# Kernel tuning notes

Measured on AMD Instinct MI355X. Metric: run time of the kernel, lower is better.

## Reference

```python
import jax, jax.numpy as jnp
import numpy as np

CH = 128
GROUPS = 8
EPS = 1e-5

def group_norm(x, w, b):
    B, C, H, W = x.shape
    g = x.reshape(B, GROUPS, C // GROUPS, H, W)
    mean = g.mean(axis=(2, 3, 4), keepdims=True)
    var = g.var(axis=(2, 3, 4), keepdims=True)
    g = (g - mean) * jax.lax.rsqrt(var + EPS)
    g = g.reshape(B, C, H, W)
    return g * w[None, :, None, None] + b[None, :, None, None]

def setup_inputs() -> dict:
    key = jax.random.key(0)
    ks = jax.random.split(key, 7)
    C = CH
    x = jax.random.normal(ks[0], (8, C, 64, 64), dtype=jnp.float32)
    gn_w = jnp.ones((C,), dtype=jnp.float32)
    gn_b = jnp.zeros((C,), dtype=jnp.float32)
    s = 1.0 / np.sqrt(C)
    qkv_w = jax.random.normal(ks[1], (3 * C, C), dtype=jnp.float32) * s
    qkv_b = jax.random.normal(ks[2], (3 * C,), dtype=jnp.float32) * 0.01
    proj_w = jax.random.normal(ks[3], (C, C), dtype=jnp.float32) * s
    proj_b = jax.random.normal(ks[4], (C,), dtype=jnp.float32) * 0.01
    return {"x": x, "gn_w": gn_w, "gn_b": gn_b, "qkv_w": qkv_w,
            "qkv_b": qkv_b, "proj_w": proj_w, "proj_b": proj_b}

def reference(x, gn_w, gn_b, qkv_w, qkv_b, proj_w, proj_b):
    B, C, H, W = x.shape
    h = group_norm(x, gn_w, gn_b)
    # 1x1 conv == per-pixel matmul over channels
    qkv = jnp.einsum('bchw,oc->bohw', h, qkv_w) + qkv_b[None, :, None, None]
    q, k, v = jnp.split(qkv.reshape(B, 3 * C, H * W), 3, axis=1)  # each [B,C,N]
    scale = C ** (-0.5)
    attn = jax.nn.softmax(jnp.einsum('bci,bcj->bij', q * scale, k), axis=-1)
    out = jnp.einsum('bij,bcj->bci', attn, v).reshape(B, C, H, W)
    out = jnp.einsum('bchw,oc->bohw', out, proj_w) + proj_b[None, :, None, None]
    return x + out
```

## Files before the change

### kernel.cpp

```cpp
#include <hip/hip_runtime.h>
#include <stdint.h>


typedef __attribute__((ext_vector_type(8))) short short8;
typedef __attribute__((ext_vector_type(4))) float f32x4;
typedef __attribute__((ext_vector_type(16))) float f32x16;

#define MFMA_BF16(a, b, c) __builtin_amdgcn_mfma_f32_16x16x32_bf16((a), (b), (c), 0, 0, 0)
#define MFMA32(a, b, c) __builtin_amdgcn_mfma_f32_32x32x16_bf16((a), (b), (c), 0, 0, 0)
#define EXP2(x) __builtin_amdgcn_exp2f(x)

#define QSCALE 0.12751743f

__device__ __forceinline__ unsigned short f2bf(float f) {
    unsigned int u = __builtin_bit_cast(unsigned int, f);
    u += 0x7FFFu + ((u >> 16) & 1u);
    return (unsigned short)(u >> 16);
}
__device__ __forceinline__ float bf2f(unsigned int lo16) {
    return __builtin_bit_cast(float, lo16 << 16);
}
__device__ __forceinline__ short8 ldg8(const unsigned short* p) {
    return __builtin_bit_cast(short8, *(const uint4*)p);
}

__global__ __launch_bounds__(256) void k_pre(const float* __restrict__ x,
                                             float* __restrict__ sums,
                                             const float* __restrict__ qkv_w,
                                             const float* __restrict__ proj_w,
                                             unsigned short* __restrict__ wq,
                                             unsigned short* __restrict__ wp) {
    if (blockIdx.x >= 1024) {
        int i = ((blockIdx.x - 1024) * 256 + threadIdx.x) * 4;
        const float* src; unsigned short* dst; int off;
        if (i < 49152) { src = qkv_w; dst = wq; off = i; }
        else           { src = proj_w; dst = wp; off = i - 49152; }
        float4 v = *(const float4*)(src + off);
        uint2 pk;
        pk.x = (unsigned int)f2bf(v.x) | ((unsigned int)f2bf(v.y) << 16);
        pk.y = (unsigned int)f2bf(v.z) | ((unsigned int)f2bf(v.w) << 16);
        *(uint2*)(dst + off) = pk;
        return;
    }
    int g     = blockIdx.x >> 4;
    int slice = blockIdx.x & 15;
    const float* p = x + (size_t)g * 65536 + slice * 4096;
    float s = 0.f, sq = 0.f;
#pragma unroll
    for (int i = 0; i < 4; ++i) {
        float4 v = *(const float4*)(p + threadIdx.x * 4 + i * 1024);
        s  += v.x + v.y + v.z + v.w;
        sq += v.x*v.x + v.y*v.y + v.z*v.z + v.w*v.w;
    }
#pragma unroll
    for (int m = 1; m < 64; m <<= 1) { s += __shfl_xor(s, m, 64); sq += __shfl_xor(sq, m, 64); }
    __shared__ float ss[4], ssq[4];
    int w = threadIdx.x >> 6;
    if ((threadIdx.x & 63) == 0) { ss[w] = s; ssq[w] = sq; }
    __syncthreads();
    if (threadIdx.x == 0) {
        atomicAdd(&sums[g * 2],     ss[0] + ss[1] + ss[2] + ss[3]);
        atomicAdd(&sums[g * 2 + 1], ssq[0] + ssq[1] + ssq[2] + ssq[3]);
    }
}

__global__ __launch_bounds__(256) void k_qkv(const float* __restrict__ x,
                                             const float* __restrict__ sums,
                                             const float* __restrict__ gn_w,
                                             const float* __restrict__ gn_b,
                                             const unsigned short* __restrict__ wq,
                                             const float* __restrict__ qkv_b,
                                             unsigned short* __restrict__ q_ws,
                                             unsigned short* __restrict__ k_ws,
                                             unsigned short* __restrict__ v_ws) {
    __shared__ unsigned short h_lds[64][136];
    const int tid  = threadIdx.x;
    const int b    = blockIdx.x >> 6;
    const int n0   = (blockIdx.x & 63) << 6;
    const int lane = tid & 63, wave = tid >> 6;
    const int l15  = lane & 15, q4 = lane >> 4;

    {
        int cb = tid >> 4;
        int nn = (tid & 15) << 2;
#pragma unroll
        for (int k = 0; k < 8; ++k) {
            int c = cb + (k << 4);
            float4 v = *(const float4*)(x + ((size_t)(b * 128 + c) << 12) + n0 + nn);
            int g = c >> 4;
            float ts = sums[(b * 8 + g) * 2];
            float tq = sums[(b * 8 + g) * 2 + 1];
            float mean = ts * (1.f / 65536.f);
            float var  = tq * (1.f / 65536.f) - mean * mean;
            float rstd = rsqrtf(var + 1e-5f);
            float ga = gn_w[c] * rstd;
            float be = gn_b[c] - mean * ga;
            h_lds[nn + 0][c] = f2bf(v.x * ga + be);
            h_lds[nn + 1][c] = f2bf(v.y * ga + be);
            h_lds[nn + 2][c] = f2bf(v.z * ga + be);
            h_lds[nn + 3][c] = f2bf(v.w * ga + be);
        }
    }
    __syncthreads();

    short8 bfrag[4][4];
#pragma unroll
    for (int nt = 0; nt < 4; ++nt)
#pragma unroll
        for (int ks = 0; ks < 4; ++ks)
            bfrag[nt][ks] = *(const short8*)&h_lds[nt * 16 + l15][ks * 32 + q4 * 8];

#pragma unroll
    for (int ot = 0; ot < 6; ++ot) {
        int o0 = wave * 96 + ot * 16;
        short8 af[4];
#pragma unroll
        for (int ks = 0; ks < 4; ++ks)
            af[ks] = ldg8(wq + (size_t)(o0 + l15) * 128 + ks * 32 + q4 * 8);

        if (o0 < 256) {
            float bias[4];
#pragma unroll
            for (int r = 0; r < 4; ++r) bias[r] = qkv_b[o0 + q4 * 4 + r];
            float qs = (o0 < 128) ? QSCALE : 1.0f;
#pragma unroll
            for (int nt = 0; nt < 4; ++nt) {
                f32x4 acc = {0.f, 0.f, 0.f, 0.f};
#pragma unroll
                for (int ks = 0; ks < 4; ++ks)
                    acc = MFMA_BF16(af[ks], bfrag[nt][ks], acc);
                int n = n0 + nt * 16 + l15;
                unsigned short* dst = (o0 < 128) ? q_ws : k_ws;
                int oo = (o0 < 128) ? o0 : (o0 - 128);
                unsigned int lo = (unsigned int)f2bf((acc[0] + bias[0]) * qs) |
                                  ((unsigned int)f2bf((acc[1] + bias[1]) * qs) << 16);
                unsigned int hi = (unsigned int)f2bf((acc[2] + bias[2]) * qs) |
                                  ((unsigned int)f2bf((acc[3] + bias[3]) * qs) << 16);
                uint2 pk; pk.x = lo; pk.y = hi;
                *(uint2*)&dst[((size_t)(b * 4096 + n) << 7) + oo + q4 * 4] = pk;
            }
        } else {
            int c = o0 - 256 + l15;
            float vb = qkv_b[o0 + l15];
            unsigned short* vrow = v_ws + ((size_t)(b * 128 + c) << 12) + n0;
#pragma unroll
            for (int nt = 0; nt < 4; ++nt) {
                f32x4 acc = {0.f, 0.f, 0.f, 0.f};
#pragma unroll
                for (int ks = 0; ks < 4; ++ks)
                    acc = MFMA_BF16(bfrag[nt][ks], af[ks], acc);
                unsigned int lo = (unsigned int)f2bf(acc[0] + vb) |
                                  ((unsigned int)f2bf(acc[1] + vb) << 16);
                unsigned int hi = (unsigned int)f2bf(acc[2] + vb) |
                                  ((unsigned int)f2bf(acc[3] + vb) << 16);
                uint2 pk; pk.x = lo; pk.y = hi;
                *(uint2*)&vrow[nt * 16 + q4 * 4] = pk;
            }
        }
    }
}

__global__ __launch_bounds__(256, 3) void k_attn_part(const unsigned short* __restrict__ q_ws,
                                                      const unsigned short* __restrict__ k_ws,
                                                      const unsigned short* __restrict__ v_ws,
                                                      unsigned short* __restrict__ o_part,
                                                      float* __restrict__ ml) {
    __shared__ unsigned short K_lds[64][136];
    __shared__ unsigned short V_lds[128][72];
    __shared__ unsigned short P_lds[64][72];

    const int tid   = threadIdx.x;
    const int chunk = blockIdx.x & 3;
    const int tile  = (blockIdx.x >> 2) & 63;
    const int b     = blockIdx.x >> 8;
    const int i0    = tile << 6;
    const int lane  = tid & 63, wave = tid >> 6;
    const int ih    = wave >> 1, jh = wave & 1;
    const int l31   = lane & 31, h = lane >> 5;

    const short8 ones = {(short)0x3F80, (short)0x3F80, (short)0x3F80, (short)0x3F80,
                         (short)0x3F80, (short)0x3F80, (short)0x3F80, (short)0x3F80};

    short8 qf[8];
    {
        const unsigned short* qp =
            q_ws + ((size_t)(b * 4096 + i0 + ih * 32 + l31) << 7) + h * 8;
#pragma unroll
        for (int ks = 0; ks < 8; ++ks) qf[ks] = ldg8(qp + ks * 16);
    }

    f32x16 acc[2];
    f32x16 lacc;
#pragma unroll
    for (int e = 0; e < 16; ++e) { lacc[e] = 0.f; acc[0][e] = 0.f; acc[1][e] = 0.f; }

    const unsigned short* kbase = k_ws + ((size_t)b << 19);
    const unsigned short* vsrc  = v_ws + ((size_t)b << 19) +
                                  ((size_t)(tid >> 1) << 12) + (tid & 1) * 32;

    for (int it = 0; it < 16; ++it) {
        int j0 = (chunk << 10) + (it << 6);
        __syncthreads();
        {
            const unsigned short* ksrc = kbase + ((size_t)j0 << 7);
#pragma unroll
            for (int i = 0; i < 4; ++i) {
                int f = i * 256 + tid;
                int row = f >> 4, q = (f & 15) << 3;
                *(uint4*)&K_lds[row][q] = *(const uint4*)(ksrc + f * 8);
            }
            const unsigned short* vp = vsrc + j0;
            uint4* vd = (uint4*)&V_lds[tid >> 1][(tid & 1) * 32];
#pragma unroll
            for (int k = 0; k < 4; ++k) vd[k] = *(const uint4*)(vp + k * 8);
        }
        __syncthreads();

        f32x16 s;
#pragma unroll
        for (int e = 0; e < 16; ++e) s[e] = 0.f;
#pragma unroll
        for (int ks = 0; ks < 8; ++ks) {
            short8 kf = *(const short8*)&K_lds[jh * 32 + l31][ks * 16 + h * 8];
            s = MFMA32(kf, qf[ks], s);
        }

        unsigned short* prow = &P_lds[ih * 32 + l31][jh * 32 + (h << 2)];
#pragma unroll
        for (int rr = 0; rr < 4; ++rr) {
            unsigned int lo = (unsigned int)f2bf(EXP2(fminf(s[rr * 4 + 0], 30.f))) |
                              ((unsigned int)f2bf(EXP2(fminf(s[rr * 4 + 1], 30.f))) << 16);
            unsigned int hi = (unsigned int)f2bf(EXP2(fminf(s[rr * 4 + 2], 30.f))) |
                              ((unsigned int)f2bf(EXP2(fminf(s[rr * 4 + 3], 30.f))) << 16);
            uint2 pk; pk.x = lo; pk.y = hi;
            *(uint2*)(prow + rr * 8) = pk;
        }
        __syncthreads();

#pragma unroll
        for (int ks = 0; ks < 4; ++ks) {
            short8 pf = *(const short8*)&P_lds[ih * 32 + l31][ks * 16 + h * 8];
            lacc = MFMA32(pf, ones, lacc);
#pragma unroll
            for (int ct = 0; ct < 2; ++ct) {
                short8 vf = *(const short8*)&V_lds[jh * 64 + ct * 32 + l31][ks * 16 + h * 8];
                acc[ct] = MFMA32(pf, vf, acc[ct]);
            }
        }
    }

    size_t pbase = (size_t)((b * 64 + tile) * 4 + chunk) * 8192;
    float rl[16];
#pragma unroll
    for (int r = 0; r < 16; ++r) rl[r] = 1.0f / lacc[r];
#pragma unroll
    for (int ct = 0; ct < 2; ++ct)
#pragma unroll
        for (int r = 0; r < 16; ++r) {
            int row = ih * 32 + (r & 3) + ((r >> 2) << 3) + (h << 2);
            o_part[pbase + (size_t)row * 128 + jh * 64 + ct * 32 + l31] =
                f2bf(acc[ct][r] * rl[r]);
        }
    if (l31 == 0 && jh == 0) {
        int mb = ((b * 64 + tile) * 4 + chunk) * 64;
#pragma unroll
        for (int r = 0; r < 16; ++r)
            ml[mb + ih * 32 + (r & 3) + ((r >> 2) << 3) + (h << 2)] = __log2f(lacc[r]);
    }
}

__global__ __launch_bounds__(256) void k_merge_proj(const unsigned short* __restrict__ o_part,
                                                    const float* __restrict__ ml,
                                                    const float* __restrict__ x,
                                                    const unsigned short* __restrict__ wp,
                                                    const float* __restrict__ proj_b,
                                                    float* __restrict__ out) {
    __shared__ unsigned short O_lds[64][136];
    __shared__ float wgt[64][4];
    const int tid  = threadIdx.x;
    const int b    = blockIdx.x >> 6;
    const int tile = blockIdx.x & 63;
    const int i0   = tile << 6;
    const int lane = tid & 63, wave = tid >> 6;
    const int l15  = lane & 15, q4 = lane >> 4;
    const int tb   = (b * 64 + tile) * 4;

    if (tid < 64) {
        float m0 = ml[(tb + 0) * 64 + tid], m1 = ml[(tb + 1) * 64 + tid];
        float m2 = ml[(tb + 2) * 64 + tid], m3 = ml[(tb + 3) * 64 + tid];
        float M = fmaxf(fmaxf(m0, m1), fmaxf(m2, m3));
        float w0 = EXP2(m0 - M), w1 = EXP2(m1 - M), w2 = EXP2(m2 - M), w3 = EXP2(m3 - M);
        float rW = 1.0f / (w0 + w1 + w2 + w3);
        wgt[tid][0] = w0 * rW; wgt[tid][1] = w1 * rW;
        wgt[tid][2] = w2 * rW; wgt[tid][3] = w3 * rW;
    }
    __syncthreads();

    {
        int n = tid >> 2, q = tid & 3;
        float w[4];
#pragma unroll
        for (int ch = 0; ch < 4; ++ch) w[ch] = wgt[n][ch];
#pragma unroll
        for (int g = 0; g < 4; ++g) {
            float acc[8];
#pragma unroll
            for (int e = 0; e < 8; ++e) acc[e] = 0.f;
#pragma unroll
            for (int ch = 0; ch < 4; ++ch) {
                const unsigned short* p =
                    o_part + (size_t)(tb + ch) * 8192 + (size_t)n * 128 + q * 32 + g * 8;
                uint4 v = *(const uint4*)p;
                float wc = w[ch];
                acc[0] += wc * bf2f(v.x & 0xFFFF); acc[1] += wc * bf2f(v.x >> 16);
                acc[2] += wc * bf2f(v.y & 0xFFFF); acc[3] += wc * bf2f(v.y >> 16);
                acc[4] += wc * bf2f(v.z & 0xFFFF); acc[5] += wc * bf2f(v.z >> 16);
                acc[6] += wc * bf2f(v.w & 0xFFFF); acc[7] += wc * bf2f(v.w >> 16);
            }
            uint4 pk;
            pk.x = (unsigned int)f2bf(acc[0]) | ((unsigned int)f2bf(acc[1]) << 16);
            pk.y = (unsigned int)f2bf(acc[2]) | ((unsigned int)f2bf(acc[3]) << 16);
            pk.z = (unsigned int)f2bf(acc[4]) | ((unsigned int)f2bf(acc[5]) << 16);
            pk.w = (unsigned int)f2bf(acc[6]) | ((unsigned int)f2bf(acc[7]) << 16);
            *(uint4*)&O_lds[n][q * 32 + g * 8] = pk;
        }
    }
    __syncthreads();

    short8 bfrag[4][4];
#pragma unroll
    for (int nt = 0; nt < 4; ++nt)
#pragma unroll
        for (int ks = 0; ks < 4; ++ks)
            bfrag[nt][ks] = *(const short8*)&O_lds[nt * 16 + l15][ks * 32 + q4 * 8];

#pragma unroll
    for (int ot = 0; ot < 2; ++ot) {
        int o0 = wave * 32 + ot * 16;
        short8 af[4];
#pragma unroll
        for (int ks = 0; ks < 4; ++ks)
            af[ks] = ldg8(wp + (size_t)(o0 + l15) * 128 + ks * 32 + q4 * 8);
        float pb[4];
#pragma unroll
        for (int r = 0; r < 4; ++r) pb[r] = proj_b[o0 + q4 * 4 + r];

#pragma unroll
        for (int nt = 0; nt < 4; ++nt) {
            f32x4 acc = {0.f, 0.f, 0.f, 0.f};
#pragma unroll
            for (int ks = 0; ks < 4; ++ks)
                acc = MFMA_BF16(af[ks], bfrag[nt][ks], acc);
#pragma unroll
            for (int r = 0; r < 4; ++r) {
                size_t idx = ((size_t)(b * 128 + o0 + q4 * 4 + r) << 12) + i0 + nt * 16 + l15;
                out[idx] = x[idx] + acc[r] + pb[r];
            }
        }
    }
}

extern "C" void kernel_launch(void* const* d_in, const int* in_sizes, int n_in,
                              void* d_out, int out_size, void* d_ws, size_t ws_size,
                              hipStream_t stream) {
    const float* x      = (const float*)d_in[0];
    const float* gn_w   = (const float*)d_in[1];
    const float* gn_b   = (const float*)d_in[2];
    const float* qkv_w  = (const float*)d_in[3];
    const float* qkv_b  = (const float*)d_in[4];
    const float* proj_w = (const float*)d_in[5];
    const float* proj_b = (const float*)d_in[6];
    float* out = (float*)d_out;

    char* ws = (char*)d_ws;
    float* sums           = (float*)ws;
    unsigned short* wq    = (unsigned short*)(ws + 4096);
    unsigned short* wp    = (unsigned short*)(ws + 4096 + 98304);
    unsigned short* q_ws  = (unsigned short*)(ws + ((size_t)1  << 20));
    unsigned short* k_ws  = (unsigned short*)(ws + ((size_t)9  << 20));
    unsigned short* v_ws  = (unsigned short*)(ws + ((size_t)17 << 20));
    unsigned short* o_part= (unsigned short*)(ws + ((size_t)25 << 20));
    float* ml             = (float*)(ws + ((size_t)57 << 20));

    hipMemsetAsync(sums, 0, 512, stream);
    k_pre<<<1088, 256, 0, stream>>>(x, sums, qkv_w, proj_w, wq, wp);
    k_qkv<<<512, 256, 0, stream>>>(x, sums, gn_w, gn_b, wq, qkv_b, q_ws, k_ws, v_ws);
    k_attn_part<<<2048, 256, 0, stream>>>(q_ws, k_ws, v_ws, o_part, ml);
    k_merge_proj<<<512, 256, 0, stream>>>(o_part, ml, x, wp, proj_b, out);
}
```

Baseline: 216.2 us.

## Restructure attention inner loop with double-buffered K, register P and split-j reduction

```diff
diff --git a/kernel.cpp b/kernel.cpp
--- a/kernel.cpp
+++ b/kernel.cpp
@@ -22,6 +22,16 @@
 }
 __device__ __forceinline__ short8 ldg8(const unsigned short* p) {
     return __builtin_bit_cast(short8, *(const uint4*)p);
+}
+__device__ __forceinline__ unsigned int cvtpk(float lo, float hi) {
+    unsigned int r;
+    asm("v_cvt_pk_bf16_f32 %0, %1, %2" : "=v"(r) : "v"(lo), "v"(hi));
+    return r;
+}
+__device__ __forceinline__ void gload16(const void* g, void* l) {
+    __builtin_amdgcn_global_load_lds(
+        (__attribute__((address_space(1))) void*)g,
+        (__attribute__((address_space(3))) void*)l, 16, 0, 0);
 }
 
 __global__ __launch_bounds__(256) void k_pre(const float* __restrict__ x,
@@ -165,9 +175,9 @@
                                                       const unsigned short* __restrict__ v_ws,
                                                       unsigned short* __restrict__ o_part,
                                                       float* __restrict__ ml) {
-    __shared__ unsigned short K_lds[64][136];
+    __shared__ unsigned short K0[64][128];
+    __shared__ unsigned short K1[64][128];
     __shared__ unsigned short V_lds[128][72];
-    __shared__ unsigned short P_lds[64][72];
 
     const int tid   = threadIdx.x;
     const int chunk = blockIdx.x & 3;
@@ -178,9 +188,6 @@
     const int ih    = wave >> 1, jh = wave & 1;
     const int l31   = lane & 31, h = lane >> 5;
 
-    const short8 ones = {(short)0x3F80, (short)0x3F80, (short)0x3F80, (short)0x3F80,
-                         (short)0x3F80, (short)0x3F80, (short)0x3F80, (short)0x3F80};
-
     short8 qf[8];
     {
         const unsigned short* qp =
@@ -189,83 +196,144 @@
         for (int ks = 0; ks < 8; ++ks) qf[ks] = ldg8(qp + ks * 16);
     }
 
-    f32x16 acc[2];
-    f32x16 lacc;
-#pragma unroll
-    for (int e = 0; e < 16; ++e) { lacc[e] = 0.f; acc[0][e] = 0.f; acc[1][e] = 0.f; }
-
-    const unsigned short* kbase = k_ws + ((size_t)b << 19);
+    f32x16 acc[4];
+#pragma unroll
+    for (int ct = 0; ct < 4; ++ct)
+#pragma unroll
+        for (int e = 0; e < 16; ++e) acc[ct][e] = 0.f;
+    float l_run = 0.f;
+
+    const unsigned short* kbase = k_ws + ((size_t)b << 19) + ((size_t)chunk << 17);
     const unsigned short* vsrc  = v_ws + ((size_t)b << 19) +
-                                  ((size_t)(tid >> 1) << 12) + (tid & 1) * 32;
-
-    for (int it = 0; it < 16; ++it) {
-        int j0 = (chunk << 10) + (it << 6);
-        __syncthreads();
-        {
-            const unsigned short* ksrc = kbase + ((size_t)j0 << 7);
-#pragma unroll
-            for (int i = 0; i < 4; ++i) {
-                int f = i * 256 + tid;
-                int row = f >> 4, q = (f & 15) << 3;
-                *(uint4*)&K_lds[row][q] = *(const uint4*)(ksrc + f * 8);
-            }
-            const unsigned short* vp = vsrc + j0;
-            uint4* vd = (uint4*)&V_lds[tid >> 1][(tid & 1) * 32];
-#pragma unroll
-            for (int k = 0; k < 4; ++k) vd[k] = *(const uint4*)(vp + k * 8);
-        }
-        __syncthreads();
-
-        f32x16 s;
-#pragma unroll
-        for (int e = 0; e < 16; ++e) s[e] = 0.f;
-#pragma unroll
-        for (int ks = 0; ks < 8; ++ks) {
-            short8 kf = *(const short8*)&K_lds[jh * 32 + l31][ks * 16 + h * 8];
-            s = MFMA32(kf, qf[ks], s);
-        }
-
-        unsigned short* prow = &P_lds[ih * 32 + l31][jh * 32 + (h << 2)];
-#pragma unroll
-        for (int rr = 0; rr < 4; ++rr) {
-            unsigned int lo = (unsigned int)f2bf(EXP2(fminf(s[rr * 4 + 0], 30.f))) |
-                              ((unsigned int)f2bf(EXP2(fminf(s[rr * 4 + 1], 30.f))) << 16);
-            unsigned int hi = (unsigned int)f2bf(EXP2(fminf(s[rr * 4 + 2], 30.f))) |
-                              ((unsigned int)f2bf(EXP2(fminf(s[rr * 4 + 3], 30.f))) << 16);
-            uint2 pk; pk.x = lo; pk.y = hi;
-            *(uint2*)(prow + rr * 8) = pk;
-        }
-        __syncthreads();
-
-#pragma unroll
-        for (int ks = 0; ks < 4; ++ks) {
-            short8 pf = *(const short8*)&P_lds[ih * 32 + l31][ks * 16 + h * 8];
-            lacc = MFMA32(pf, ones, lacc);
-#pragma unroll
-            for (int ct = 0; ct < 2; ++ct) {
-                short8 vf = *(const short8*)&V_lds[jh * 64 + ct * 32 + l31][ks * 16 + h * 8];
-                acc[ct] = MFMA32(pf, vf, acc[ct]);
-            }
-        }
-    }
-
-    size_t pbase = (size_t)((b * 64 + tile) * 4 + chunk) * 8192;
-    float rl[16];
-#pragma unroll
-    for (int r = 0; r < 16; ++r) rl[r] = 1.0f / lacc[r];
-#pragma unroll
-    for (int ct = 0; ct < 2; ++ct)
+                                  ((size_t)(tid >> 1) << 12) + (tid & 1) * 32 +
+                                  (chunk << 10);
+
+    int srcChunk[4];
+#pragma unroll
+    for (int q = 0; q < 4; ++q) {
+        int c   = wave * 256 + q * 64 + lane;
+        int row = c >> 4;
+        srcChunk[q] = row * 16 + ((c & 15) ^ (row & 15));
+    }
+    const int krow = jh * 32 + l31;
+    const int ksw  = krow & 15;
+
+#pragma unroll
+    for (int q = 0; q < 4; ++q)
+        gload16(kbase + srcChunk[q] * 8, (char*)(&K0[0][0]) + wave * 4096 + q * 1024);
+    uint4 vregs[4];
+#pragma unroll
+    for (int k = 0; k < 4; ++k) vregs[k] = *(const uint4*)(vsrc + k * 8);
+
+#define ATTN_ITER(IT, KR, KP)                                                         \
+  do {                                                                                \
+    __syncthreads();        \
+    {                                                                                 \
+      uint4* vd = (uint4*)&V_lds[tid >> 1][(tid & 1) * 32];                           \
+      vd[0] = vregs[0]; vd[1] = vregs[1]; vd[2] = vregs[2]; vd[3] = vregs[3];         \
+    }                                                                                 \
+    __syncthreads();                             \
+    if ((IT) < 15) {       \
+      const unsigned short* kt = kbase + ((IT) + 1) * 8192;                           \
+      char* kd = (char*)(&KP[0][0]) + wave * 4096;                                    \
+      _Pragma("unroll")                                                               \
+      for (int q = 0; q < 4; ++q) gload16(kt + srcChunk[q] * 8, kd + q * 1024);       \
+      const unsigned short* vp = vsrc + ((IT) + 1) * 64;                              \
+      _Pragma("unroll")                                                               \
+      for (int k = 0; k < 4; ++k) vregs[k] = *(const uint4*)(vp + k * 8);             \
+    }                                                                                 \
+    f32x16 s;           \
+    _Pragma("unroll")                                                                 \
+    for (int e = 0; e < 16; ++e) s[e] = 0.f;                                          \
+    __builtin_amdgcn_s_setprio(1);                                                    \
+    _Pragma("unroll")                                                                 \
+    for (int ks = 0; ks < 8; ++ks) {                                                  \
+      short8 kf = *(const short8*)&KR[krow][((ks * 2 + h) ^ ksw) << 3];               \
+      s = MFMA32(kf, qf[ks], s);                                                      \
+    }                                                                                 \
+    __builtin_amdgcn_s_setprio(0);                                                    \
+    float p[16];                       \
+    _Pragma("unroll")                                                                 \
+    for (int e = 0; e < 16; ++e) p[e] = EXP2(fminf(s[e], 30.f));                      \
+    l_run += (((p[0] + p[1]) + (p[2] + p[3])) + ((p[4] + p[5]) + (p[6] + p[7]))) +    \
+             (((p[8] + p[9]) + (p[10] + p[11])) + ((p[12] + p[13]) + (p[14] + p[15])));\
+    short8 paf[2];                \
+    _Pragma("unroll")                                                                 \
+    for (int ks = 0; ks < 2; ++ks) {                                                  \
+      const float* pp = p + ks * 8;                                                   \
+      unsigned int Wa = cvtpk(pp[0], pp[1]);      \
+      unsigned int Wc = cvtpk(pp[2], pp[3]);               \
+      unsigned int Wb = cvtpk(pp[4], pp[5]);               \
+      unsigned int Wd = cvtpk(pp[6], pp[7]);               \
+            \
+      auto r1 = __builtin_amdgcn_permlane32_swap(Wa, Wb, false, false);               \
+      auto r2 = __builtin_amdgcn_permlane32_swap(Wc, Wd, false, false);               \
+           \
+           \
+      uint4 aw; aw.x = r1[0]; aw.y = r2[0]; aw.z = r1[1]; aw.w = r2[1];               \
+      paf[ks] = __builtin_bit_cast(short8, aw);                                       \
+    }                                                                                 \
+    __builtin_amdgcn_s_setprio(1);                                                    \
+    _Pragma("unroll")                                                                 \
+    for (int ks = 0; ks < 2; ++ks)                                                    \
+      _Pragma("unroll")                                                               \
+      for (int ct = 0; ct < 4; ++ct) {                                                \
+        short8 vf = *(const short8*)&V_lds[ct * 32 + l31][jh * 32 + ks * 16 + h * 8]; \
+        acc[ct] = MFMA32(paf[ks], vf, acc[ct]);                                       \
+      }                                                                               \
+    __builtin_amdgcn_s_setprio(0);                                                    \
+  } while (0)
+
+    for (int ib = 0; ib < 8; ++ib) {
+        ATTN_ITER(ib * 2,     K0, K1);
+        ATTN_ITER(ib * 2 + 1, K1, K0);
+    }
+#undef ATTN_ITER
+
+    __syncthreads();
+    float* Ob0 = (float*)(&K0[0][0]);
+    float* Ob1 = (float*)(&K1[0][0]);
+    float* Lp  = (float*)(&V_lds[0][0]);
+    float l2 = l_run + __shfl_xor(l_run, 32);
+    Lp[jh * 64 + ih * 32 + l31] = l2;
+    {
+        float* Ob = jh ? Ob0 : Ob1;
+#pragma unroll
+        for (int cc = 0; cc < 2; ++cc) {
+            int ct = jh ? cc : cc + 2;
+#pragma unroll
+            for (int r = 0; r < 16; ++r) {
+                int il = (r & 3) + ((r >> 2) << 3) + (h << 2);
+                Ob[(ih * 32 + il) * 64 + cc * 32 + l31] = acc[ct][r];
+            }
+        }
+    }
+    __syncthreads();
+    {
+        size_t pbase = (size_t)((b * 64 + tile) * 4 + chunk) * 8192;
+        float rl[16];
 #pragma unroll
         for (int r = 0; r < 16; ++r) {
-            int row = ih * 32 + (r & 3) + ((r >> 2) << 3) + (h << 2);
-            o_part[pbase + (size_t)row * 128 + jh * 64 + ct * 32 + l31] =
-                f2bf(acc[ct][r] * rl[r]);
-        }
-    if (l31 == 0 && jh == 0) {
-        int mb = ((b * 64 + tile) * 4 + chunk) * 64;
-#pragma unroll
-        for (int r = 0; r < 16; ++r)
-            ml[mb + ih * 32 + (r & 3) + ((r >> 2) << 3) + (h << 2)] = __log2f(lacc[r]);
+            int il = (r & 3) + ((r >> 2) << 3) + (h << 2);
+            rl[r] = 1.0f / (Lp[ih * 32 + il] + Lp[64 + ih * 32 + il]);
+        }
+        float* Ob = jh ? Ob1 : Ob0;
+#pragma unroll
+        for (int cc = 0; cc < 2; ++cc) {
+            int ct = jh ? cc + 2 : cc;
+#pragma unroll
+            for (int r = 0; r < 16; ++r) {
+                int il = (r & 3) + ((r >> 2) << 3) + (h << 2);
+                float v = acc[ct][r] + Ob[(ih * 32 + il) * 64 + cc * 32 + l31];
+                o_part[pbase + (size_t)(ih * 32 + il) * 128 + ct * 32 + l31] =
+                    f2bf(v * rl[r]);
+            }
+        }
+        if (jh == 0 && lane < 32) {
+            int mb = ((b * 64 + tile) * 4 + chunk) * 64;
+            ml[mb + ih * 32 + lane] =
+                __log2f(Lp[ih * 32 + lane] + Lp[64 + ih * 32 + lane]);
+        }
     }
 }
 
```

After: 616.3 us. 185% more time.
